# Kernel tuning notes

Measured on AMD Instinct MI355X. Metric: run time of the kernel, lower is better.

## Reference

```python
import jax, jax.numpy as jnp
import numpy as np

N_WIRES = 22
DEPTH = 1


def _apply_ry(state, theta, wire):
    # RY(theta) = [[cos(t/2), -sin(t/2)], [sin(t/2), cos(t/2)]] (torchquantum convention)
    c = jnp.cos(theta * 0.5).astype(jnp.complex64)
    s = jnp.sin(theta * 0.5).astype(jnp.complex64)
    st = jnp.moveaxis(state, wire, 0)  # [2, 2^(n-1) ...]
    new = jnp.stack([c * st[0] - s * st[1], s * st[0] + c * st[1]])
    return jnp.moveaxis(new, 0, wire)


def _apply_cnot(state, ctrl, tgt):
    st = jnp.moveaxis(state, (ctrl, tgt), (0, 1))
    st = st.at[1].set(st[1, ::-1])  # flip target where control == 1
    return jnp.moveaxis(st, (0, 1), (ctrl, tgt))


def _encode(angles, n_wires=N_WIRES, depth=DEPTH):
    # start in |0...0>
    state = jnp.zeros((2,) * n_wires, dtype=jnp.complex64).at[(0,) * n_wires].set(1.0 + 0.0j)
    for w in range(n_wires):
        state = _apply_ry(state, angles[w], w)
    for _ in range(depth):
        for i in range(n_wires):
            state = _apply_cnot(state, i, (i + 1) % n_wires)
    return state


def setup_inputs() -> dict:
    key = jax.random.key(0)
    kx, ky = jax.random.split(key)
    x = jax.random.normal(kx, (N_WIRES,), dtype=jnp.float32)
    y = jax.random.normal(ky, (N_WIRES,), dtype=jnp.float32)
    return {"x": x, "y": y}


def reference(x, y):
    n = N_WIRES
    psi_x = _encode(x)  # state1 in the torch code
    psi_y = _encode(y)
    # torch does: states_y @ states_x.conj() on tensors of shape [1, 2, ..., 2]
    # -> batched 2x2 matmul over the leading n-1 qubit axes, then abs().view(-1)
    shape = (1,) + (2,) * n
    overlap = jnp.matmul(psi_y.reshape(shape), jnp.conj(psi_x).reshape(shape))
    return jnp.abs(overlap).reshape(-1)
```

## Files before the change

### kernel.cpp

```cpp
#include <hip/hip_runtime.h>
#include <math.h>


__global__ __launch_bounds__(256) void qk_precompute(
    const float* __restrict__ x, const float* __restrict__ y,
    float* __restrict__ ws)
{
    __shared__ float f[2][44];
    const int t = threadIdx.x;
    if (t < 22) {
        float sv, cv;
        sincosf(0.5f * x[t], &sv, &cv);
        f[0][2 * t] = cv; f[0][2 * t + 1] = sv;
        sincosf(0.5f * y[t], &sv, &cv);
        f[1][2 * t] = cv; f[1][2 * t + 1] = sv;
    }
    __syncthreads();

    const int e   = blockIdx.x * 256 + t;
    const int tbl = e >> 9;
    const int i   = e & 511;
    const float* F = f[tbl & 1];
    float prod = 1.0f;
    if (tbl < 2) {
#pragma unroll
        for (int q = 0; q < 9; ++q) prod *= F[2 * (10 - q) + ((i >> q) & 1)];
    } else {
#pragma unroll
        for (int p = 0; p < 9; ++p) prod *= F[2 * (19 - p) + ((i >> p) & 1)];
    }
    ws[e] = prod;

    if (blockIdx.x == 0 && t < 8) {
        const int s0 = (t >> 2) & 1, s1 = (t >> 1) & 1, s19 = t & 1;
#pragma unroll
        for (int ii = 0; ii < 2; ++ii) {
#pragma unroll
            for (int j = 0; j < 2; ++j) {
                float sum = 0.0f;
#pragma unroll
                for (int k = 0; k < 2; ++k) {
                    float kx = f[0][s0 ^ j] * f[0][2 + (s1 ^ s0 ^ j)]
                             * f[0][40 + (k ^ s19)] * f[0][42 + (j ^ k)];
                    float ky = f[1][s0 ^ k] * f[1][2 + (s1 ^ s0 ^ k)]
                             * f[1][40 + (ii ^ s19)] * f[1][42 + (k ^ ii)];
                    sum += ky * kx;
                }
                ws[2048 + 4 * t + 2 * ii + j] = fabsf(sum);
            }
        }
    }
}

__global__ __launch_bounds__(256) void qk_main(
    const float* __restrict__ ws, float* __restrict__ out)
{
    const unsigned b  = blockIdx.x * 256u + threadIdx.x;
    const unsigned g  = b ^ (b >> 1);
    const unsigned i2 = g & 511u;
    const unsigned i1 = (g >> 9) & 511u;
    const float coreX = ws[i1]        * ws[1024u + i2];
    const float coreY = ws[512u + i1] * ws[1536u + i2];
    const float p = fabsf(coreX * coreY);
    const unsigned m = ((b >> 17) & 6u) | (b & 1u);
    const float4 a = reinterpret_cast<const float4*>(ws + 2048)[m];
    float4 o;
    o.x = p * a.x; o.y = p * a.y; o.z = p * a.z; o.w = p * a.w;
    reinterpret_cast<float4*>(out)[b] = o;
}

extern "C" void kernel_launch(void* const* d_in, const int* in_sizes, int n_in,
                              void* d_out, int out_size, void* d_ws, size_t ws_size,
                              hipStream_t stream) {
    const float* x = (const float*)d_in[0];
    const float* y = (const float*)d_in[1];
    float* ws  = (float*)d_ws;
    float* out = (float*)d_out;
    qk_precompute<<<8, 256, 0, stream>>>(x, y, ws);
    const unsigned n_b = 1u << 20;
    qk_main<<<n_b / 256, 256, 0, stream>>>(ws, out);
}
```

Measured before the change: 63.95 us.

## Fuse precompute and main kernels with per-block shared-memory tables

Merges the two launches into one kernel. Each block recomputes the sincos factors and builds product tables in shared memory, precombining x and y factors into a single 512-entry pair of tables. Each thread then writes four float4 outputs, so 1024 blocks cover the full output. This removes one kernel launch and the global workspace round trip, at the cost of redundant table setup and extra barriers in every block.

```diff
diff --git a/kernel.cpp b/kernel.cpp
--- a/kernel.cpp
+++ b/kernel.cpp
@@ -2,36 +2,43 @@
 #include <math.h>
 
 
-__global__ __launch_bounds__(256) void qk_precompute(
+#define BLOCKS 1024
+#define QPT 4
+
+__global__ __launch_bounds__(256) void qk_fused(
     const float* __restrict__ x, const float* __restrict__ y,
-    float* __restrict__ ws)
+    float* __restrict__ out)
 {
-    __shared__ float f[2][44];
+    __shared__ float fx[44], fy[44], h[44];
+    __shared__ float U1[512], U2[512];
+    __shared__ float absM[32];
     const int t = threadIdx.x;
+
     if (t < 22) {
         float sv, cv;
         sincosf(0.5f * x[t], &sv, &cv);
-        f[0][2 * t] = cv; f[0][2 * t + 1] = sv;
+        fx[2 * t] = cv; fx[2 * t + 1] = sv;
         sincosf(0.5f * y[t], &sv, &cv);
-        f[1][2 * t] = cv; f[1][2 * t + 1] = sv;
+        fy[2 * t] = cv; fy[2 * t + 1] = sv;
     }
     __syncthreads();
+    if (t < 44) h[t] = fx[t] * fy[t];
+    __syncthreads();
 
-    const int e   = blockIdx.x * 256 + t;
-    const int tbl = e >> 9;
-    const int i   = e & 511;
-    const float* F = f[tbl & 1];
-    float prod = 1.0f;
-    if (tbl < 2) {
 #pragma unroll
-        for (int q = 0; q < 9; ++q) prod *= F[2 * (10 - q) + ((i >> q) & 1)];
-    } else {
+    for (int r = 0; r < 2; ++r) {
+        const int i = t + 256 * r;
+        float p1 = 1.0f, p2 = 1.0f;
 #pragma unroll
-        for (int p = 0; p < 9; ++p) prod *= F[2 * (19 - p) + ((i >> p) & 1)];
+        for (int q = 0; q < 9; ++q) {
+            const int bit = (i >> q) & 1;
+            p1 *= h[2 * (10 - q) + bit];
+            p2 *= h[2 * (19 - q) + bit];
+        }
+        U1[i] = fabsf(p1);
+        U2[i] = fabsf(p2);
     }
-    ws[e] = prod;
-
-    if (blockIdx.x == 0 && t < 8) {
+    if (t < 8) {
         const int s0 = (t >> 2) & 1, s1 = (t >> 1) & 1, s19 = t & 1;
 #pragma unroll
         for (int ii = 0; ii < 2; ++ii) {
@@ -40,33 +47,30 @@
                 float sum = 0.0f;
 #pragma unroll
                 for (int k = 0; k < 2; ++k) {
-                    float kx = f[0][s0 ^ j] * f[0][2 + (s1 ^ s0 ^ j)]
-                             * f[0][40 + (k ^ s19)] * f[0][42 + (j ^ k)];
-                    float ky = f[1][s0 ^ k] * f[1][2 + (s1 ^ s0 ^ k)]
-                             * f[1][40 + (ii ^ s19)] * f[1][42 + (k ^ ii)];
+                    float kx = fx[s0 ^ j] * fx[2 + (s1 ^ s0 ^ j)]
+                             * fx[40 + (k ^ s19)] * fx[42 + (j ^ k)];
+                    float ky = fy[s0 ^ k] * fy[2 + (s1 ^ s0 ^ k)]
+                             * fy[40 + (ii ^ s19)] * fy[42 + (k ^ ii)];
                     sum += ky * kx;
                 }
-                ws[2048 + 4 * t + 2 * ii + j] = fabsf(sum);
+                absM[4 * t + 2 * ii + j] = fabsf(sum);
             }
         }
     }
-}
+    __syncthreads();
 
-__global__ __launch_bounds__(256) void qk_main(
-    const float* __restrict__ ws, float* __restrict__ out)
-{
-    const unsigned b  = blockIdx.x * 256u + threadIdx.x;
-    const unsigned g  = b ^ (b >> 1);
-    const unsigned i2 = g & 511u;
-    const unsigned i1 = (g >> 9) & 511u;
-    const float coreX = ws[i1]        * ws[1024u + i2];
-    const float coreY = ws[512u + i1] * ws[1536u + i2];
-    const float p = fabsf(coreX * coreY);
-    const unsigned m = ((b >> 17) & 6u) | (b & 1u);
-    const float4 a = reinterpret_cast<const float4*>(ws + 2048)[m];
-    float4 o;
-    o.x = p * a.x; o.y = p * a.y; o.z = p * a.z; o.w = p * a.w;
-    reinterpret_cast<float4*>(out)[b] = o;
+    const unsigned base = blockIdx.x * (256u * QPT);
+#pragma unroll
+    for (int k = 0; k < QPT; ++k) {
+        const unsigned b = base + k * 256u + (unsigned)t;
+        const unsigned g = b ^ (b >> 1);
+        const float p = U1[(g >> 9) & 511u] * U2[g & 511u];
+        const unsigned m = ((b >> 17) & 6u) | (b & 1u);
+        const float4 a = reinterpret_cast<const float4*>(absM)[m];
+        float4 o;
+        o.x = p * a.x; o.y = p * a.y; o.z = p * a.z; o.w = p * a.w;
+        reinterpret_cast<float4*>(out)[b] = o;
+    }
 }
 
 extern "C" void kernel_launch(void* const* d_in, const int* in_sizes, int n_in,
@@ -74,9 +78,6 @@
                               hipStream_t stream) {
     const float* x = (const float*)d_in[0];
     const float* y = (const float*)d_in[1];
-    float* ws  = (float*)d_ws;
     float* out = (float*)d_out;
-    qk_precompute<<<8, 256, 0, stream>>>(x, y, ws);
-    const unsigned n_b = 1u << 20;
-    qk_main<<<n_b / 256, 256, 0, stream>>>(ws, out);
+    qk_fused<<<BLOCKS, 256, 0, stream>>>(x, y, out);
 }
```

Measured after the change: 61.98 us. 1.03x faster.
